# Performance work log

Hardware: AMD Instinct MI355X
Metric: run time of the kernel (lower is better)

The kernel has to match this reference:

```python
import jax, jax.numpy as jnp
import numpy as np

B, T, D, H, L = 65536, 8, 60, 128, 64


def _lstm_layer(x, Wih, Whh, bih, bhh):
    """Single LSTM layer, batch_first. x: [B,T,Din]. Returns (ys [B,T,H], h_last [B,H]).
    PyTorch gate order: i, f, g, o."""
    Bsz = x.shape[0]
    Hd = Whh.shape[1]
    # Precompute input contribution for all timesteps: [B,T,4H]
    xg = jnp.einsum('btd,gd->btg', x, Wih) + bih + bhh

    def step(carry, xt):
        h, c = carry
        g = xt + h @ Whh.T  # [B,4H]
        i, f, gg, o = jnp.split(g, 4, axis=-1)
        i = jax.nn.sigmoid(i)
        f = jax.nn.sigmoid(f)
        gg = jnp.tanh(gg)
        o = jax.nn.sigmoid(o)
        c = f * c + i * gg
        h = o * jnp.tanh(c)
        return (h, c), h

    h0 = jnp.zeros((Bsz, Hd), x.dtype)
    c0 = jnp.zeros((Bsz, Hd), x.dtype)
    (h_last, _), ys = jax.lax.scan(step, (h0, c0), jnp.swapaxes(xg, 0, 1))
    return jnp.swapaxes(ys, 0, 1), h_last


def setup_inputs() -> dict:
    key = jax.random.key(0)
    ks = jax.random.split(key, 24)
    s = 1.0 / np.sqrt(H)  # torch LSTM/Linear default uniform bound

    def u(k, shape):
        return jax.random.uniform(k, shape, jnp.float32, -s, s)

    inp = {"x": jax.random.normal(ks[0], (B, T, D), jnp.float32)}
    # encoder layer 0 (in=D), layer 1 (in=H); decoder layer 0 (in=L), layer 1 (in=H)
    dims = {"enc0": D, "enc1": H, "dec0": L, "dec1": H}
    i = 1
    for name, din in dims.items():
        inp[name + "_Wih"] = u(ks[i], (4 * H, din)); i += 1
        inp[name + "_Whh"] = u(ks[i], (4 * H, H)); i += 1
        inp[name + "_bih"] = u(ks[i], (4 * H,)); i += 1
        inp[name + "_bhh"] = u(ks[i], (4 * H,)); i += 1
    inp["W_lat"] = u(ks[i], (L, H)); i += 1
    inp["b_lat"] = u(ks[i], (L,)); i += 1
    inp["W_out"] = jax.random.uniform(ks[i], (D, H), jnp.float32, -s, s); i += 1
    inp["b_out"] = jax.random.uniform(ks[i], (D,), jnp.float32, -s, s)
    return inp


def reference(x,
              enc0_Wih, enc0_Whh, enc0_bih, enc0_bhh,
              enc1_Wih, enc1_Whh, enc1_bih, enc1_bhh,
              dec0_Wih, dec0_Whh, dec0_bih, dec0_bhh,
              dec1_Wih, dec1_Whh, dec1_bih, dec1_bhh,
              W_lat, b_lat, W_out, b_out):
    # Encoder (eval mode: inter-layer dropout is identity)
    h1, _ = _lstm_layer(x, enc0_Wih, enc0_Whh, enc0_bih, enc0_bhh)
    _, h_last = _lstm_layer(h1, enc1_Wih, enc1_Whh, enc1_bih, enc1_bhh)
    # Latent bottleneck from top-layer final hidden state
    z = h_last @ W_lat.T + b_lat  # [B,L]
    z_seq = jnp.broadcast_to(z[:, None, :], (z.shape[0], T, z.shape[1]))
    # Decoder
    d1, _ = _lstm_layer(z_seq, dec0_Wih, dec0_Whh, dec0_bih, dec0_bhh)
    d2, _ = _lstm_layer(d1, dec1_Wih, dec1_Whh, dec1_bih, dec1_bhh)
    recon = jnp.einsum('bth,dh->btd', d2, W_out) + b_out  # [B,T,D]
    return recon
```

## Files before the change

### kernel.cpp

```cpp
#include <hip/hip_runtime.h>

typedef _Float16 f16;
typedef _Float16 f16x8 __attribute__((ext_vector_type(8)));
typedef float    f32x4 __attribute__((ext_vector_type(4)));

#define MFMA16(a,b,c) __builtin_amdgcn_mfma_f32_16x16x32_f16(a,b,c,0,0,0)

#define HIST_S 1096
#define HB_S   136
#define HB_BUF 4352

__device__ __forceinline__ float sigm(float v){
  return __builtin_amdgcn_rcpf(1.f + __builtin_amdgcn_exp2f(-1.4426950408889634f*v));
}
__device__ __forceinline__ float tanha(float v){
  return 1.f - 2.f*__builtin_amdgcn_rcpf(1.f + __builtin_amdgcn_exp2f(2.8853900817779268f*v));
}
__device__ __forceinline__ f32x4 splat4(float v){ f32x4 r; r[0]=v;r[1]=v;r[2]=v;r[3]=v; return r; }

__device__ __forceinline__ f16x8 ldfrag(const float* __restrict__ W, int K, int n, int k0){
  const float* p = W + n*K + k0;
  f32x4 a = *(const f32x4*)p;
  f32x4 b = *(const f32x4*)(p+4);
  f16x8 r;
  #pragma unroll
  for (int i=0;i<4;i++){ r[i] = (f16)a[i]; r[4+i] = (f16)b[i]; }
  return r;
}
__device__ __forceinline__ f16x8 ldfrag60(const float* __restrict__ W, int n, int k0){
  const float* p = W + n*60 + k0;
  f32x4 a = *(const f32x4*)p;
  f16x8 r;
  #pragma unroll
  for (int i=0;i<4;i++) r[i] = (f16)a[i];
  if (k0 < 56){
    f32x4 b = *(const f32x4*)(p+4);
    #pragma unroll
    for (int i=0;i<4;i++) r[4+i] = (f16)b[i];
  } else {
    #pragma unroll
    for (int i=0;i<4;i++) r[4+i] = (f16)0.f;
  }
  return r;
}
__device__ __forceinline__ f16x8 zfrag(){
  f16x8 r;
  #pragma unroll
  for (int i=0;i<8;i++) r[i] = (f16)0.f;
  return r;
}

__device__ __forceinline__ void act_update(f32x4 acc[2][4], f32x4* cst, f16* dst, int stride, int col, int qd){
  #pragma unroll
  for (int m=0;m<2;m++){
    #pragma unroll
    for (int r=0;r<4;r++){
      float ii = sigm(acc[m][0][r]);
      float ff = sigm(acc[m][1][r]);
      float gg = tanha(acc[m][2][r]);
      float oo = sigm(acc[m][3][r]);
      float cn = ff*cst[m][r] + ii*gg;
      cst[m][r] = cn;
      dst[(m*16+qd*4+r)*stride + col] = (f16)(oo*tanha(cn));
    }
  }
}

__global__ void __launch_bounds__(512, 2)
lstm_main(const float* __restrict__ x,
          const float* __restrict__ e0Wih, const float* __restrict__ e0Whh, const float* __restrict__ e0bi, const float* __restrict__ e0bh,
          const float* __restrict__ e1Wih, const float* __restrict__ e1Whh, const float* __restrict__ e1bi, const float* __restrict__ e1bh,
          const float* __restrict__ d0Wih, const float* __restrict__ d0Whh, const float* __restrict__ d0bi, const float* __restrict__ d0bh,
          const float* __restrict__ d1Wih, const float* __restrict__ d1Whh, const float* __restrict__ d1bi, const float* __restrict__ d1bh,
          const float* __restrict__ Wlat,  const float* __restrict__ blat,
          const float* __restrict__ Wout,  const float* __restrict__ bout,
          float* __restrict__ out)
{
  __shared__ __align__(16) f16 hist[32*HIST_S];
  __shared__ __align__(16) f16 hb1 [HB_BUF];

  const int tid = threadIdx.x;
  const int w   = tid >> 6;
  const int ln  = tid & 15;
  const int qd  = (tid >> 4) & 3;
  const int bs  = blockIdx.x << 5;
  const int col = w*16 + ln;

  f16x8 Bf[4][8];
  f32x4 acc[2][4];
  f32x4 cst[2];
  float bg[4];

  #pragma unroll
  for (int g=0;g<4;g++){
    const int n = g*128 + col;
    #pragma unroll
    for (int kb=0;kb<2;kb++) Bf[g][kb]   = ldfrag60(e0Wih, n, kb*32 + qd*8);
    #pragma unroll
    for (int kb=0;kb<4;kb++) Bf[g][kb+2] = ldfrag(e0Whh, 128, n, kb*32 + qd*8);
    bg[g] = e0bi[n] + e0bh[n];
  }
  cst[0] = splat4(0.f); cst[1] = splat4(0.f);
  for (int t=0; t<8; t++){
    #pragma unroll
    for (int m=0;m<2;m++)
      #pragma unroll
      for (int g=0;g<4;g++) acc[m][g] = splat4(bg[g]);
    #pragma unroll
    for (int kb=0; kb<2; kb++){
      #pragma unroll
      for (int m=0;m<2;m++){
        const float* p = x + (bs + m*16 + ln)*480 + t*60 + kb*32 + qd*8;
        f16x8 a;
        {
          f32x4 lo = *(const f32x4*)p;
          #pragma unroll
          for (int i=0;i<4;i++) a[i] = (f16)lo[i];
          if (kb==1 && qd==3){
            #pragma unroll
            for (int i=0;i<4;i++) a[4+i] = (f16)0.f;
          } else {
            f32x4 hi = *(const f32x4*)(p+4);
            #pragma unroll
            for (int i=0;i<4;i++) a[4+i] = (f16)hi[i];
          }
        }
        #pragma unroll
        for (int g=0; g<4; g++) acc[m][g] = MFMA16(a, Bf[g][kb], acc[m][g]);
      }
    }
    if (t > 0){
      #pragma unroll
      for (int kb=0; kb<4; kb++){
        #pragma unroll
        for (int m=0;m<2;m++){
          f16x8 a = *(const f16x8*)(hist + (m*16+ln)*HIST_S + (t-1)*HB_S + kb*32 + qd*8);
          #pragma unroll
          for (int g=0; g<4; g++) acc[m][g] = MFMA16(a, Bf[g][kb+2], acc[m][g]);
        }
      }
    }
    act_update(acc, cst, hist + t*HB_S, HIST_S, col, qd);
    __syncthreads();
  }

  #pragma unroll
  for (int g=0;g<4;g++){
    const int n = g*128 + col;
    #pragma unroll
    for (int kb=0;kb<4;kb++){
      Bf[g][kb]   = ldfrag(e1Wih, 128, n, kb*32 + qd*8);
      Bf[g][kb+4] = ldfrag(e1Whh, 128, n, kb*32 + qd*8);
    }
    bg[g] = e1bi[n] + e1bh[n];
  }
  cst[0] = splat4(0.f); cst[1] = splat4(0.f);
  for (int t=0; t<8; t++){
    #pragma unroll
    for (int m=0;m<2;m++)
      #pragma unroll
      for (int g=0;g<4;g++) acc[m][g] = splat4(bg[g]);
    #pragma unroll
    for (int kb=0; kb<4; kb++){
      #pragma unroll
      for (int m=0;m<2;m++){
        f16x8 a = *(const f16x8*)(hist + (m*16+ln)*HIST_S + t*HB_S + kb*32 + qd*8);
        #pragma unroll
        for (int g=0; g<4; g++) acc[m][g] = MFMA16(a, Bf[g][kb], acc[m][g]);
      }
    }
    if (t > 0){
      #pragma unroll
      for (int kb=0; kb<4; kb++){
        #pragma unroll
        for (int m=0;m<2;m++){
          f16x8 a = *(const f16x8*)(hb1 + (m*16+ln)*HB_S + kb*32 + qd*8);
          #pragma unroll
          for (int g=0; g<4; g++) acc[m][g] = MFMA16(a, Bf[g][kb+4], acc[m][g]);
        }
      }
    }
    __syncthreads();
    act_update(acc, cst, hb1, HB_S, col, qd);
    __syncthreads();
  }

  {
    const int mo = w & 1, no = w >> 1;
    const int zn = no*16 + ln;
    f32x4 zacc = splat4(blat[zn]);
    f16x8 Bz[4];
    #pragma unroll
    for (int kb=0;kb<4;kb++) Bz[kb] = ldfrag(Wlat, 128, zn, kb*32 + qd*8);
    #pragma unroll
    for (int kb=0;kb<4;kb++){
      f16x8 a = *(const f16x8*)(hb1 + (mo*16+ln)*HB_S + kb*32 + qd*8);
      zacc = MFMA16(a, Bz[kb], zacc);
    }
    __syncthreads();
    #pragma unroll
    for (int r=0;r<4;r++)
      hb1[(mo*16+qd*4+r)*HB_S + zn] = (f16)zacc[r];
  }
  __syncthreads();

  f32x4 xga[2][4];
  {
    f16x8 Bd[4][2];
    #pragma unroll
    for (int g=0;g<4;g++){
      const int n = g*128 + col;
      #pragma unroll
      for (int kb=0;kb<2;kb++) Bd[g][kb] = ldfrag(d0Wih, 64, n, kb*32 + qd*8);
      float bgd = d0bi[n] + d0bh[n];
      xga[0][g] = splat4(bgd); xga[1][g] = splat4(bgd);
    }
    #pragma unroll
    for (int kb=0; kb<2; kb++){
      #pragma unroll
      for (int m=0;m<2;m++){
        f16x8 a = *(const f16x8*)(hb1 + (m*16+ln)*HB_S + kb*32 + qd*8);
        #pragma unroll
        for (int g=0; g<4; g++) xga[m][g] = MFMA16(a, Bd[g][kb], xga[m][g]);
      }
    }
  }

  #pragma unroll
  for (int g=0;g<4;g++){
    const int n = g*128 + col;
    #pragma unroll
    for (int kb=0;kb<4;kb++) Bf[g][kb] = ldfrag(d0Whh, 128, n, kb*32 + qd*8);
  }
  cst[0] = splat4(0.f); cst[1] = splat4(0.f);
  for (int t=0; t<8; t++){
    #pragma unroll
    for (int m=0;m<2;m++)
      #pragma unroll
      for (int g=0;g<4;g++) acc[m][g] = xga[m][g];
    if (t > 0){
      #pragma unroll
      for (int kb=0; kb<4; kb++){
        #pragma unroll
        for (int m=0;m<2;m++){
          f16x8 a = *(const f16x8*)(hist + (m*16+ln)*HIST_S + (t-1)*HB_S + kb*32 + qd*8);
          #pragma unroll
          for (int g=0; g<4; g++) acc[m][g] = MFMA16(a, Bf[g][kb], acc[m][g]);
        }
      }
    }
    act_update(acc, cst, hist + t*HB_S, HIST_S, col, qd);
    __syncthreads();
  }

  #pragma unroll
  for (int g=0;g<4;g++){
    const int n = g*128 + col;
    #pragma unroll
    for (int kb=0;kb<4;kb++){
      Bf[g][kb]   = ldfrag(d1Wih, 128, n, kb*32 + qd*8);
      Bf[g][kb+4] = ldfrag(d1Whh, 128, n, kb*32 + qd*8);
    }
    bg[g] = d1bi[n] + d1bh[n];
  }
  const int dcol = (w>>1)*16 + ln;
  const int mo   = w & 1;
  f16x8 BO[4];
  #pragma unroll
  for (int kb=0;kb<4;kb++)
    BO[kb] = (dcol < 60) ? ldfrag(Wout, 128, dcol, kb*32 + qd*8) : zfrag();
  const float bo = (dcol < 60) ? bout[dcol] : 0.f;
  cst[0] = splat4(0.f); cst[1] = splat4(0.f);
  for (int t=0; t<8; t++){
    #pragma unroll
    for (int m=0;m<2;m++)
      #pragma unroll
      for (int g=0;g<4;g++) acc[m][g] = splat4(bg[g]);
    #pragma unroll
    for (int kb=0; kb<4; kb++){
      #pragma unroll
      for (int m=0;m<2;m++){
        f16x8 a = *(const f16x8*)(hist + (m*16+ln)*HIST_S + t*HB_S + kb*32 + qd*8);
        #pragma unroll
        for (int g=0; g<4; g++) acc[m][g] = MFMA16(a, Bf[g][kb], acc[m][g]);
      }
    }
    if (t > 0){
      #pragma unroll
      for (int kb=0; kb<4; kb++){
        #pragma unroll
        for (int m=0;m<2;m++){
          f16x8 a = *(const f16x8*)(hb1 + (m*16+ln)*HB_S + kb*32 + qd*8);
          #pragma unroll
          for (int g=0; g<4; g++) acc[m][g] = MFMA16(a, Bf[g][kb+4], acc[m][g]);
        }
      }
    }
    __syncthreads();
    act_update(acc, cst, hb1, HB_S, col, qd);
    __syncthreads();
    f32x4 ao = splat4(bo);
    const f16* hb2 = hb1 + (mo*16+ln)*HB_S + qd*8;
    #pragma unroll
    for (int kb=0; kb<4; kb++){
      f16x8 a = *(const f16x8*)(hb2 + kb*32);
      ao = MFMA16(a, BO[kb], ao);
    }
    if (dcol < 60){
      #pragma unroll
      for (int r=0;r<4;r++){
        int s = mo*16 + qd*4 + r;
        out[(bs + s)*480 + t*60 + dcol] = ao[r];
      }
    }
  }
}

extern "C" void kernel_launch(void* const* d_in, const int* in_sizes, int n_in,
                              void* d_out, int out_size, void* d_ws, size_t ws_size,
                              hipStream_t stream)
{
  (void)d_ws; (void)ws_size; (void)in_sizes; (void)n_in; (void)out_size;
  hipLaunchKernelGGL(lstm_main, dim3(2048), dim3(512), 0, stream,
                     (const float*)d_in[0],
                     (const float*)d_in[1],  (const float*)d_in[2],  (const float*)d_in[3],  (const float*)d_in[4],
                     (const float*)d_in[5],  (const float*)d_in[6],  (const float*)d_in[7],  (const float*)d_in[8],
                     (const float*)d_in[9],  (const float*)d_in[10], (const float*)d_in[11], (const float*)d_in[12],
                     (const float*)d_in[13], (const float*)d_in[14], (const float*)d_in[15], (const float*)d_in[16],
                     (const float*)d_in[17], (const float*)d_in[18],
                     (const float*)d_in[19], (const float*)d_in[20],
                     (float*)d_out);
}
```

Before: 1.249 ms.

## Split LSTM gates across paired wave groups with 1024-thread blocks

Each block now runs 16 waves instead of 8. Waves are paired by gate: one half computes the i/f gates and the other computes g/o, so each wave holds half the weight fragments and accumulators. The g/o half applies tanh/sigmoid and passes the results through a new fp32 LDS scratch buffer, and the i/f half then updates the cell and hidden state. The goal is to roughly halve per-thread register pressure for the weight fragments and spread the MFMA work over more waves. The cost is an extra barrier and LDS round-trip every timestep, uneven activation work between the two halves, and higher LDS use per block, which allows only one block per CU.

```diff
diff --git a/kernel.cpp b/kernel.cpp
--- a/kernel.cpp
+++ b/kernel.cpp
@@ -3,12 +3,14 @@
 typedef _Float16 f16;
 typedef _Float16 f16x8 __attribute__((ext_vector_type(8)));
 typedef float    f32x4 __attribute__((ext_vector_type(4)));
+typedef float    f32x2 __attribute__((ext_vector_type(2)));
 
 #define MFMA16(a,b,c) __builtin_amdgcn_mfma_f32_16x16x32_f16(a,b,c,0,0,0)
 
 #define HIST_S 1096
 #define HB_S   136
 #define HB_BUF 4352
+#define SGS    260
 
 __device__ __forceinline__ float sigm(float v){
   return __builtin_amdgcn_rcpf(1.f + __builtin_amdgcn_exp2f(-1.4426950408889634f*v));
@@ -50,23 +52,37 @@
   return r;
 }
 
-__device__ __forceinline__ void act_update(f32x4 acc[2][4], f32x4* cst, f16* dst, int stride, int col, int qd){
+__device__ __forceinline__ void write_go(f32x4 acc[2][2], float* sc, int col, int qd){
   #pragma unroll
   for (int m=0;m<2;m++){
     #pragma unroll
     for (int r=0;r<4;r++){
+      int s = m*16 + qd*4 + r;
+      f32x2 v; v[0] = tanha(acc[m][0][r]); v[1] = sigm(acc[m][1][r]);
+      *(f32x2*)&sc[s*SGS + col*2] = v;
+    }
+  }
+}
+
+__device__ __forceinline__ void act_update_split(f32x4 acc[2][2], f32x4* cst,
+                                                 const float* sc, f16* dst, int stride,
+                                                 int col, int qd){
+  #pragma unroll
+  for (int m=0;m<2;m++){
+    #pragma unroll
+    for (int r=0;r<4;r++){
+      int s = m*16 + qd*4 + r;
+      f32x2 go = *(const f32x2*)&sc[s*SGS + col*2];
       float ii = sigm(acc[m][0][r]);
       float ff = sigm(acc[m][1][r]);
-      float gg = tanha(acc[m][2][r]);
-      float oo = sigm(acc[m][3][r]);
-      float cn = ff*cst[m][r] + ii*gg;
+      float cn = ff*cst[m][r] + ii*go[0];
       cst[m][r] = cn;
-      dst[(m*16+qd*4+r)*stride + col] = (f16)(oo*tanha(cn));
-    }
-  }
-}
-
-__global__ void __launch_bounds__(512, 2)
+      dst[s*stride + col] = (f16)(go[1]*tanha(cn));
+    }
+  }
+}
+
+__global__ void __launch_bounds__(1024, 1)
 lstm_main(const float* __restrict__ x,
           const float* __restrict__ e0Wih, const float* __restrict__ e0Whh, const float* __restrict__ e0bi, const float* __restrict__ e0bh,
           const float* __restrict__ e1Wih, const float* __restrict__ e1Whh, const float* __restrict__ e1bi, const float* __restrict__ e1bh,
@@ -76,36 +92,40 @@
           const float* __restrict__ Wout,  const float* __restrict__ bout,
           float* __restrict__ out)
 {
-  __shared__ __align__(16) f16 hist[32*HIST_S];
-  __shared__ __align__(16) f16 hb1 [HB_BUF];
+  __shared__ __align__(16) f16   hist[32*HIST_S];
+  __shared__ __align__(16) f16   hb1 [HB_BUF];
+  __shared__ __align__(16) float gsc [32*SGS];
 
   const int tid = threadIdx.x;
   const int w   = tid >> 6;
   const int ln  = tid & 15;
   const int qd  = (tid >> 4) & 3;
   const int bs  = blockIdx.x << 5;
-  const int col = w*16 + ln;
-
-  f16x8 Bf[4][8];
-  f32x4 acc[2][4];
+  const int gp  = w & 1;
+  const int cs  = w >> 1;
+  const int col = cs*16 + ln;
+  const int g0  = gp*2;
+
+  f16x8 Bf[2][8];
+  f32x4 acc[2][2];
   f32x4 cst[2];
-  float bg[4];
-
-  #pragma unroll
-  for (int g=0;g<4;g++){
-    const int n = g*128 + col;
-    #pragma unroll
-    for (int kb=0;kb<2;kb++) Bf[g][kb]   = ldfrag60(e0Wih, n, kb*32 + qd*8);
-    #pragma unroll
-    for (int kb=0;kb<4;kb++) Bf[g][kb+2] = ldfrag(e0Whh, 128, n, kb*32 + qd*8);
-    bg[g] = e0bi[n] + e0bh[n];
+  float bg[2];
+
+  #pragma unroll
+  for (int gi=0; gi<2; gi++){
+    const int n = (g0+gi)*128 + col;
+    #pragma unroll
+    for (int kb=0;kb<2;kb++) Bf[gi][kb]   = ldfrag60(e0Wih, n, kb*32 + qd*8);
+    #pragma unroll
+    for (int kb=0;kb<4;kb++) Bf[gi][kb+2] = ldfrag(e0Whh, 128, n, kb*32 + qd*8);
+    bg[gi] = e0bi[n] + e0bh[n];
   }
   cst[0] = splat4(0.f); cst[1] = splat4(0.f);
   for (int t=0; t<8; t++){
     #pragma unroll
     for (int m=0;m<2;m++)
       #pragma unroll
-      for (int g=0;g<4;g++) acc[m][g] = splat4(bg[g]);
+      for (int gi=0;gi<2;gi++) acc[m][gi] = splat4(bg[gi]);
     #pragma unroll
     for (int kb=0; kb<2; kb++){
       #pragma unroll
@@ -126,7 +146,7 @@
           }
         }
         #pragma unroll
-        for (int g=0; g<4; g++) acc[m][g] = MFMA16(a, Bf[g][kb], acc[m][g]);
+        for (int gi=0; gi<2; gi++) acc[m][gi] = MFMA16(a, Bf[gi][kb], acc[m][gi]);
       }
     }
     if (t > 0){
@@ -136,37 +156,39 @@
         for (int m=0;m<2;m++){
           f16x8 a = *(const f16x8*)(hist + (m*16+ln)*HIST_S + (t-1)*HB_S + kb*32 + qd*8);
           #pragma unroll
-          for (int g=0; g<4; g++) acc[m][g] = MFMA16(a, Bf[g][kb+2], acc[m][g]);
-        }
-      }
-    }
-    act_update(acc, cst, hist + t*HB_S, HIST_S, col, qd);
-    __syncthreads();
-  }
-
-  #pragma unroll
-  for (int g=0;g<4;g++){
-    const int n = g*128 + col;
+          for (int gi=0; gi<2; gi++) acc[m][gi] = MFMA16(a, Bf[gi][kb+2], acc[m][gi]);
+        }
+      }
+    }
+    if (gp) write_go(acc, gsc, col, qd);
+    __syncthreads();
+    if (!gp) act_update_split(acc, cst, gsc, hist + t*HB_S, HIST_S, col, qd);
+    __syncthreads();
+  }
+
+  #pragma unroll
+  for (int gi=0; gi<2; gi++){
+    const int n = (g0+gi)*128 + col;
     #pragma unroll
     for (int kb=0;kb<4;kb++){
-      Bf[g][kb]   = ldfrag(e1Wih, 128, n, kb*32 + qd*8);
-      Bf[g][kb+4] = ldfrag(e1Whh, 128, n, kb*32 + qd*8);
-    }
-    bg[g] = e1bi[n] + e1bh[n];
+      Bf[gi][kb]   = ldfrag(e1Wih, 128, n, kb*32 + qd*8);
+      Bf[gi][kb+4] = ldfrag(e1Whh, 128, n, kb*32 + qd*8);
+    }
+    bg[gi] = e1bi[n] + e1bh[n];
   }
   cst[0] = splat4(0.f); cst[1] = splat4(0.f);
   for (int t=0; t<8; t++){
     #pragma unroll
     for (int m=0;m<2;m++)
       #pragma unroll
-      for (int g=0;g<4;g++) acc[m][g] = splat4(bg[g]);
+      for (int gi=0;gi<2;gi++) acc[m][gi] = splat4(bg[gi]);
     #pragma unroll
     for (int kb=0; kb<4; kb++){
       #pragma unroll
       for (int m=0;m<2;m++){
         f16x8 a = *(const f16x8*)(hist + (m*16+ln)*HIST_S + t*HB_S + kb*32 + qd*8);
         #pragma unroll
-        for (int g=0; g<4; g++) acc[m][g] = MFMA16(a, Bf[g][kb], acc[m][g]);
+        for (int gi=0; gi<2; gi++) acc[m][gi] = MFMA16(a, Bf[gi][kb], acc[m][gi]);
       }
     }
     if (t > 0){
@@ -176,44 +198,49 @@
         for (int m=0;m<2;m++){
           f16x8 a = *(const f16x8*)(hb1 + (m*16+ln)*HB_S + kb*32 + qd*8);
           #pragma unroll
-          for (int g=0; g<4; g++) acc[m][g] = MFMA16(a, Bf[g][kb+4], acc[m][g]);
-        }
-      }
-    }
-    __syncthreads();
-    act_update(acc, cst, hb1, HB_S, col, qd);
+          for (int gi=0; gi<2; gi++) acc[m][gi] = MFMA16(a, Bf[gi][kb+4], acc[m][gi]);
+        }
+      }
+    }
+    if (gp) write_go(acc, gsc, col, qd);
+    __syncthreads();
+    if (!gp) act_update_split(acc, cst, gsc, hb1, HB_S, col, qd);
     __syncthreads();
   }
 
   {
-    const int mo = w & 1, no = w >> 1;
-    const int zn = no*16 + ln;
-    f32x4 zacc = splat4(blat[zn]);
-    f16x8 Bz[4];
-    #pragma unroll
-    for (int kb=0;kb<4;kb++) Bz[kb] = ldfrag(Wlat, 128, zn, kb*32 + qd*8);
-    #pragma unroll
-    for (int kb=0;kb<4;kb++){
-      f16x8 a = *(const f16x8*)(hb1 + (mo*16+ln)*HB_S + kb*32 + qd*8);
-      zacc = MFMA16(a, Bz[kb], zacc);
-    }
-    __syncthreads();
-    #pragma unroll
-    for (int r=0;r<4;r++)
-      hb1[(mo*16+qd*4+r)*HB_S + zn] = (f16)zacc[r];
-  }
-  __syncthreads();
-
-  f32x4 xga[2][4];
+    const int mo = cs & 1, zn = (cs>>1)*16 + ln;
+    f32x4 zacc;
+    if (gp){
+      zacc = splat4(blat[zn]);
+      f16x8 Bz[4];
+      #pragma unroll
+      for (int kb=0;kb<4;kb++) Bz[kb] = ldfrag(Wlat, 128, zn, kb*32 + qd*8);
+      #pragma unroll
+      for (int kb=0;kb<4;kb++){
+        f16x8 a = *(const f16x8*)(hb1 + (mo*16+ln)*HB_S + kb*32 + qd*8);
+        zacc = MFMA16(a, Bz[kb], zacc);
+      }
+    }
+    __syncthreads();
+    if (gp){
+      #pragma unroll
+      for (int r=0;r<4;r++)
+        hb1[(mo*16+qd*4+r)*HB_S + zn] = (f16)zacc[r];
+    }
+    __syncthreads();
+  }
+
+  f32x4 xga[2][2];
   {
-    f16x8 Bd[4][2];
-    #pragma unroll
-    for (int g=0;g<4;g++){
-      const int n = g*128 + col;
-      #pragma unroll
-      for (int kb=0;kb<2;kb++) Bd[g][kb] = ldfrag(d0Wih, 64, n, kb*32 + qd*8);
+    f16x8 Bd[2][2];
+    #pragma unroll
+    for (int gi=0; gi<2; gi++){
+      const int n = (g0+gi)*128 + col;
+      #pragma unroll
+      for (int kb=0;kb<2;kb++) Bd[gi][kb] = ldfrag(d0Wih, 64, n, kb*32 + qd*8);
       float bgd = d0bi[n] + d0bh[n];
-      xga[0][g] = splat4(bgd); xga[1][g] = splat4(bgd);
+      xga[0][gi] = splat4(bgd); xga[1][gi] = splat4(bgd);
     }
     #pragma unroll
     for (int kb=0; kb<2; kb++){
@@ -221,23 +248,23 @@
       for (int m=0;m<2;m++){
         f16x8 a = *(const f16x8*)(hb1 + (m*16+ln)*HB_S + kb*32 + qd*8);
         #pragma unroll
-        for (int g=0; g<4; g++) xga[m][g] = MFMA16(a, Bd[g][kb], xga[m][g]);
-      }
-    }
-  }
-
-  #pragma unroll
-  for (int g=0;g<4;g++){
-    const int n = g*128 + col;
-    #pragma unroll
-    for (int kb=0;kb<4;kb++) Bf[g][kb] = ldfrag(d0Whh, 128, n, kb*32 + qd*8);
+        for (int gi=0; gi<2; gi++) xga[m][gi] = MFMA16(a, Bd[gi][kb], xga[m][gi]);
+      }
+    }
+  }
+
+  #pragma unroll
+  for (int gi=0; gi<2; gi++){
+    const int n = (g0+gi)*128 + col;
+    #pragma unroll
+    for (int kb=0;kb<4;kb++) Bf[gi][kb] = ldfrag(d0Whh, 128, n, kb*32 + qd*8);
   }
   cst[0] = splat4(0.f); cst[1] = splat4(0.f);
   for (int t=0; t<8; t++){
     #pragma unroll
     for (int m=0;m<2;m++)
       #pragma unroll
-      for (int g=0;g<4;g++) acc[m][g] = xga[m][g];
+      for (int gi=0;gi<2;gi++) acc[m][gi] = xga[m][gi];
     if (t > 0){
       #pragma unroll
       for (int kb=0; kb<4; kb++){
@@ -245,44 +272,49 @@
         for (int m=0;m<2;m++){
           f16x8 a = *(const f16x8*)(hist + (m*16+ln)*HIST_S + (t-1)*HB_S + kb*32 + qd*8);
           #pragma unroll
-          for (int g=0; g<4; g++) acc[m][g] = MFMA16(a, Bf[g][kb], acc[m][g]);
-        }
-      }
-    }
-    act_update(acc, cst, hist + t*HB_S, HIST_S, col, qd);
-    __syncthreads();
-  }
-
-  #pragma unroll
-  for (int g=0;g<4;g++){
-    const int n = g*128 + col;
+          for (int gi=0; gi<2; gi++) acc[m][gi] = MFMA16(a, Bf[gi][kb], acc[m][gi]);
+        }
+      }
+    }
+    if (gp) write_go(acc, gsc, col, qd);
+    __syncthreads();
+    if (!gp) act_update_split(acc, cst, gsc, hist + t*HB_S, HIST_S, col, qd);
+    __syncthreads();
+  }
+
+  #pragma unroll
+  for (int gi=0; gi<2; gi++){
+    const int n = (g0+gi)*128 + col;
     #pragma unroll
     for (int kb=0;kb<4;kb++){
-      Bf[g][kb]   = ldfrag(d1Wih, 128, n, kb*32 + qd*8);
-      Bf[g][kb+4] = ldfrag(d1Whh, 128, n, kb*32 + qd*8);
-    }
-    bg[g] = d1bi[n] + d1bh[n];
-  }
-  const int dcol = (w>>1)*16 + ln;
-  const int mo   = w & 1;
+      Bf[gi][kb]   = ldfrag(d1Wih, 128, n, kb*32 + qd*8);
+      Bf[gi][kb+4] = ldfrag(d1Whh, 128, n, kb*32 + qd*8);
+    }
+    bg[gi] = d1bi[n] + d1bh[n];
+  }
+  const int mo2  = cs & 1;
+  const int dcol = (cs>>1)*16 + ln;
   f16x8 BO[4];
-  #pragma unroll
-  for (int kb=0;kb<4;kb++)
-    BO[kb] = (dcol < 60) ? ldfrag(Wout, 128, dcol, kb*32 + qd*8) : zfrag();
-  const float bo = (dcol < 60) ? bout[dcol] : 0.f;
+  float bo = 0.f;
+  if (gp){
+    #pragma unroll
+    for (int kb=0;kb<4;kb++)
+      BO[kb] = (dcol < 60) ? ldfrag(Wout, 128, dcol, kb*32 + qd*8) : zfrag();
+    bo = (dcol < 60) ? bout[dcol] : 0.f;
+  }
   cst[0] = splat4(0.f); cst[1] = splat4(0.f);
   for (int t=0; t<8; t++){
     #pragma unroll
     for (int m=0;m<2;m++)
       #pragma unroll
-      for (int g=0;g<4;g++) acc[m][g] = splat4(bg[g]);
+      for (int gi=0;gi<2;gi++) acc[m][gi] = splat4(bg[gi]);
     #pragma unroll
     for (int kb=0; kb<4; kb++){
       #pragma unroll
       for (int m=0;m<2;m++){
         f16x8 a = *(const f16x8*)(hist + (m*16+ln)*HIST_S + t*HB_S + kb*32 + qd*8);
         #pragma unroll
-        for (int g=0; g<4; g++) acc[m][g] = MFMA16(a, Bf[g][kb], acc[m][g]);
+        for (int gi=0; gi<2; gi++) acc[m][gi] = MFMA16(a, Bf[gi][kb], acc[m][gi]);
       }
     }
     if (t > 0){
@@ -292,25 +324,28 @@
         for (int m=0;m<2;m++){
           f16x8 a = *(const f16x8*)(hb1 + (m*16+ln)*HB_S + kb*32 + qd*8);
           #pragma unroll
-          for (int g=0; g<4; g++) acc[m][g] = MFMA16(a, Bf[g][kb+4], acc[m][g]);
-        }
-      }
-    }
-    __syncthreads();
-    act_update(acc, cst, hb1, HB_S, col, qd);
-    __syncthreads();
-    f32x4 ao = splat4(bo);
-    const f16* hb2 = hb1 + (mo*16+ln)*HB_S + qd*8;
-    #pragma unroll
-    for (int kb=0; kb<4; kb++){
-      f16x8 a = *(const f16x8*)(hb2 + kb*32);
-      ao = MFMA16(a, BO[kb], ao);
-    }
-    if (dcol < 60){
-      #pragma unroll
-      for (int r=0;r<4;r++){
-        int s = mo*16 + qd*4 + r;
-        out[(bs + s)*480 + t*60 + dcol] = ao[r];
+          for (int gi=0; gi<2; gi++) acc[m][gi] = MFMA16(a, Bf[gi][kb+4], acc[m][gi]);
+        }
+      }
+    }
+    if (gp) write_go(acc, gsc, col, qd);
+    __syncthreads();
+    if (!gp) act_update_split(acc, cst, gsc, hb1, HB_S, col, qd);
+    __syncthreads();
+    if (gp){
+      f32x4 ao = splat4(bo);
+      const f16* hb2 = hb1 + (mo2*16+ln)*HB_S + qd*8;
+      #pragma unroll
+      for (int kb=0; kb<4; kb++){
+        f16x8 a = *(const f16x8*)(hb2 + kb*32);
+        ao = MFMA16(a, BO[kb], ao);
+      }
+      if (dcol < 60){
+        #pragma unroll
+        for (int r=0;r<4;r++){
+          int s = mo2*16 + qd*4 + r;
+          out[(bs + s)*480 + t*60 + dcol] = ao[r];
+        }
       }
     }
   }
@@ -321,7 +356,7 @@
                               hipStream_t stream)
 {
   (void)d_ws; (void)ws_size; (void)in_sizes; (void)n_in; (void)out_size;
-  hipLaunchKernelGGL(lstm_main, dim3(2048), dim3(512), 0, stream,
+  hipLaunchKernelGGL(lstm_main, dim3(2048), dim3(1024), 0, stream,
                      (const float*)d_in[0],
                      (const float*)d_in[1],  (const float*)d_in[2],  (const float*)d_in[3],  (const float*)d_in[4],
                      (const float*)d_in[5],  (const float*)d_in[6],  (const float*)d_in[7],  (const float*)d_in[8],
```

Result: slower. 1.732 ms (+38.7%).
